# Performance work log

Hardware: AMD Instinct MI355X
Metric: run time of the kernel (lower is better)

## Reference

```python
import jax, jax.numpy as jnp
import numpy as np

VOCAB = 100000
EMB = 300
HID = 512            # bidirectional total; per-direction = 256
HD = HID // 2
TAGS = 12
START = 10
STOP = 11
NEG = -10000.0
T = 4096


def _lstm_dir(x, h0, c0, Wih, Whh, bih, bhh, reverse):
    # x: [T, EMB]; PyTorch gate order i, f, g, o
    def step(carry, xt):
        h, c = carry
        g = xt @ Wih.T + h @ Whh.T + bih + bhh           # [4*HD]
        i, f, gg, o = jnp.split(g, 4)
        i = jax.nn.sigmoid(i); f = jax.nn.sigmoid(f)
        gg = jnp.tanh(gg); o = jax.nn.sigmoid(o)
        c = f * c + i * gg
        h = o * jnp.tanh(c)
        return (h, c), h
    _, hs = jax.lax.scan(step, (h0, c0), x, reverse=reverse)
    return hs                                            # [T, HD]


def setup_inputs() -> dict:
    key = jax.random.key(0)
    ks = jax.random.split(key, 16)
    s = 0.05  # weight scale for numerical stability
    sentence = jax.random.randint(ks[0], (T,), 0, VOCAB)
    h0 = jax.random.normal(ks[1], (2, HD), jnp.float32)
    c0 = jax.random.normal(ks[2], (2, HD), jnp.float32)
    embed = jax.random.normal(ks[3], (VOCAB, EMB), jnp.float32) * s
    W_ih_f = jax.random.normal(ks[4], (4 * HD, EMB), jnp.float32) * s
    W_hh_f = jax.random.normal(ks[5], (4 * HD, HD), jnp.float32) * s
    b_ih_f = jax.random.normal(ks[6], (4 * HD,), jnp.float32) * s
    b_hh_f = jax.random.normal(ks[7], (4 * HD,), jnp.float32) * s
    W_ih_b = jax.random.normal(ks[8], (4 * HD, EMB), jnp.float32) * s
    W_hh_b = jax.random.normal(ks[9], (4 * HD, HD), jnp.float32) * s
    b_ih_b = jax.random.normal(ks[10], (4 * HD,), jnp.float32) * s
    b_hh_b = jax.random.normal(ks[11], (4 * HD,), jnp.float32) * s
    W_tag = jax.random.normal(ks[12], (TAGS, HID), jnp.float32) * s
    b_tag = jax.random.normal(ks[13], (TAGS,), jnp.float32) * s
    transitions = jax.random.normal(ks[14], (TAGS, TAGS), jnp.float32)
    transitions = transitions.at[START, :].set(NEG).at[:, STOP].set(NEG)
    return dict(sentence=sentence, h0=h0, c0=c0, embed=embed,
                W_ih_f=W_ih_f, W_hh_f=W_hh_f, b_ih_f=b_ih_f, b_hh_f=b_hh_f,
                W_ih_b=W_ih_b, W_hh_b=W_hh_b, b_ih_b=b_ih_b, b_hh_b=b_hh_b,
                W_tag=W_tag, b_tag=b_tag, transitions=transitions)


def reference(sentence, h0, c0, embed,
              W_ih_f, W_hh_f, b_ih_f, b_hh_f,
              W_ih_b, W_hh_b, b_ih_b, b_hh_b,
              W_tag, b_tag, transitions):
    # --- BiLSTM features (dropout layers are identity at inference) ---
    x = embed[sentence]                                      # [T, EMB]
    hf = _lstm_dir(x, h0[0], c0[0], W_ih_f, W_hh_f, b_ih_f, b_hh_f, False)
    hb = _lstm_dir(x, h0[1], c0[1], W_ih_b, W_hh_b, b_ih_b, b_hh_b, True)
    feats = jnp.concatenate([hf, hb], axis=-1) @ W_tag.T + b_tag  # [T, TAGS]

    # --- Viterbi decode: transitions[to, from] ---
    init = jnp.full((TAGS,), NEG, jnp.float32).at[START].set(0.0)

    def vstep(fv, feat):
        ntv = fv[None, :] + transitions                      # [to, from]
        bp = jnp.argmax(ntv, axis=1)                         # best prev tag per 'to'
        fv2 = jnp.max(ntv, axis=1) + feat
        return fv2, bp

    fv, bps = jax.lax.scan(vstep, init, feats)               # bps: [T, TAGS]
    terminal = fv + transitions[STOP]
    best = jnp.argmax(terminal)
    path_score = terminal[best]

    def back(tag, bp):
        return bp[tag], tag

    _, best_path = jax.lax.scan(back, best, bps, reverse=True)  # [T] tags in time order
    return path_score, best_path
```

## Files before the change

kernel.cpp:

```cpp
#include <hip/hip_runtime.h>

#define T_LEN 4096
#define EMB   300
#define HD    256
#define G4    1024
#define N2    2048
#define TAGS  12
#define NEGV  -10000.0f
#define SENT  0x7F7F7F7Fu
#define NLSTM 29
#define VCH   512

#define MV(K) { const float4 hv = h4[K];                    \
    a0 = fmaf(wA##K.x, hv.x, a0);                           \
    a1 = fmaf(wA##K.y, hv.y, a1);                           \
    a2 = fmaf(wA##K.z, hv.z, a2);                           \
    a3 = fmaf(wA##K.w, hv.w, a3); }

__global__ __launch_bounds__(1024) void fused_gemm_lstm(
    const int* __restrict__ sent, const float* __restrict__ embed,
    const float* __restrict__ Wihf, const float* __restrict__ Wihb,
    const float* __restrict__ bihf, const float* __restrict__ bhhf,
    const float* __restrict__ bihb, const float* __restrict__ bhhb,
    const float* Whh_f, const float* Whh_b,
    const float* __restrict__ h0, const float* __restrict__ c0,
    float* gin,
    float* Hh)
{
    __shared__ __align__(16) char smem[145*1024];
    const int blk = blockIdx.x;
    const int tid = threadIdx.x;

    if (blk >= NLSTM) {
        float* AsT  = (float*)smem;
        float* BsT  = (float*)(smem + 8704);
        int*   sIdx = (int*)  (smem + 17408);
        const int g  = blk - NLSTM;
        const int kk8 = g >> 5;
        const int bn  = g & 31;
        const int bm  = (kk8 & 1) ? (63 - (kk8 >> 1)) : (kk8 >> 1);

        if (tid < 64) sIdx[tid] = sent[bm*64 + tid];
        __syncthreads();

        const int srow = tid >> 4;
        const int skj  = (tid & 15) << 1;
        const int m0   = (tid >> 5) << 1;
        const int n0   = (tid & 31) << 1;
        const int rn   = bn * 64;
        float acc00=0.f, acc01=0.f, acc10=0.f, acc11=0.f;

        for (int kc = 0; kc < 10; ++kc) {
            const int k0 = kc*32 + skj;
            float2 va = make_float2(0.f, 0.f), vb = make_float2(0.f, 0.f);
            if (k0 + 1 < EMB) {
                va = *(const float2*)(embed + (long)sIdx[srow]*EMB + k0);
                const int r = rn + srow;
                const float* bsrc = (r < G4) ? (Wihf + (long)r*EMB)
                                             : (Wihb + (long)(r-G4)*EMB);
                vb = *(const float2*)(bsrc + k0);
            }
            AsT[skj*68 + srow]     = va.x;
            AsT[(skj+1)*68 + srow] = va.y;
            BsT[skj*68 + srow]     = vb.x;
            BsT[(skj+1)*68 + srow] = vb.y;
            __syncthreads();
            #pragma unroll
            for (int kk = 0; kk < 32; ++kk) {
                const float2 a2v = *(const float2*)&AsT[kk*68 + m0];
                const float2 b2v = *(const float2*)&BsT[kk*68 + n0];
                acc00 = fmaf(a2v.x, b2v.x, acc00);
                acc01 = fmaf(a2v.x, b2v.y, acc01);
                acc10 = fmaf(a2v.y, b2v.x, acc10);
                acc11 = fmaf(a2v.y, b2v.y, acc11);
            }
            __syncthreads();
        }

        const int c0i = rn + n0, c1i = c0i + 1;
        const float bias0 = (c0i < G4) ? (bihf[c0i] + bhhf[c0i])
                                       : (bihb[c0i-G4] + bhhb[c0i-G4]);
        const float bias1 = (c1i < G4) ? (bihf[c1i] + bhhf[c1i])
                                       : (bihb[c1i-G4] + bhhb[c1i-G4]);
        const long t0 = (long)(bm*64 + m0), t1 = t0 + 1;
        __hip_atomic_store(&gin[t0*N2 + c0i], acc00 + bias0,
                           __ATOMIC_RELAXED, __HIP_MEMORY_SCOPE_AGENT);
        __hip_atomic_store(&gin[t0*N2 + c1i], acc01 + bias1,
                           __ATOMIC_RELAXED, __HIP_MEMORY_SCOPE_AGENT);
        __hip_atomic_store(&gin[t1*N2 + c0i], acc10 + bias0,
                           __ATOMIC_RELAXED, __HIP_MEMORY_SCOPE_AGENT);
        __hip_atomic_store(&gin[t1*N2 + c1i], acc11 + bias1,
                           __ATOMIC_RELAXED, __HIP_MEMORY_SCOPE_AGENT);
        return;
    }

    const int m8 = blk & 7;
    if (m8 != 0 && m8 != 4) return;
    const int dir = (m8 == 4);
    const int b   = blk >> 3;
    const int u     = tid & 63;
    const int wvid  = tid >> 6;
    const int gate  = wvid >> 2;
    const int q     = wvid & 3;
    const int unit0 = b*64;
    const int row   = gate*64 + u;
    const int grow  = gate*HD + unit0 + u;

    float* hS  = (float*)smem;
    float* ps  = (float*)(smem + 1024);
    float* gvS = (float*)(smem + 4096);

    const float4* W4 = (const float4*)((dir ? Whh_b : Whh_f)
                                       + (long)grow*HD + q*64);
    const float4 wA0  = W4[0],  wA1  = W4[1],  wA2  = W4[2],  wA3  = W4[3];
    const float4 wA4  = W4[4],  wA5  = W4[5],  wA6  = W4[6],  wA7  = W4[7];
    const float4 wA8  = W4[8],  wA9  = W4[9],  wA10 = W4[10], wA11 = W4[11];
    const float4 wA12 = W4[12], wA13 = W4[13], wA14 = W4[14], wA15 = W4[15];

    float cst = 0.f;
    if (tid < 64) cst = c0[dir*HD + unit0 + tid];
    if (tid < HD) hS[tid] = h0[dir*HD + tid];

    float* ginD = gin + dir*G4;
    float gx;
    {
        const long gi0 = (long)(dir ? T_LEN-1 : 0)*N2 + grow;
        do {
            gx = __hip_atomic_load(&ginD[gi0], __ATOMIC_RELAXED,
                                   __HIP_MEMORY_SCOPE_AGENT);
        } while (__float_as_uint(gx) == SENT);
    }

    #pragma unroll 1
    for (int s = 0; s < T_LEN; ++s) {
        const int t = dir ? (T_LEN-1-s) : s;
        float gxn = 0.f;
        long  gidx = 0;
        if (s+1 < T_LEN) {
            gidx = (long)(dir ? t-1 : t+1)*N2 + grow;
            gxn = __hip_atomic_load(&ginD[gidx], __ATOMIC_RELAXED,
                                    __HIP_MEMORY_SCOPE_AGENT);
            __builtin_amdgcn_sched_barrier(0);
        }

        __syncthreads();
        const float4* h4 = (const float4*)(hS + q*64);
        float a0=0.f, a1=0.f, a2=0.f, a3=0.f;
        MV(0)  MV(1)  MV(2)  MV(3)
        MV(4)  MV(5)  MV(6)  MV(7)
        MV(8)  MV(9)  MV(10) MV(11)
        MV(12) MV(13) MV(14) MV(15)
        const float a = (a0+a1)+(a2+a3);
        if (q != 0) ps[(q-1)*256 + row] = a;
        __syncthreads();

        if (q == 0) {
            const float raw = a + ps[row] + ps[256+row] + ps[512+row] + gx;
            gvS[row] = (gate == 2) ? tanhf(raw) : 1.f/(1.f + expf(-raw));
        }
        __syncthreads();

        if (tid < 64) {
            const float i_ = gvS[tid],       f_ = gvS[64+tid];
            const float g_ = gvS[128+tid],   o_ = gvS[192+tid];
            cst = fmaf(f_, cst, i_*g_);
            const float hv = o_ * tanhf(cst);
            hS[unit0 + tid] = hv;
            __hip_atomic_store(&Hh[(long)t*512 + dir*HD + unit0 + tid], hv,
                               __ATOMIC_RELAXED, __HIP_MEMORY_SCOPE_AGENT);
        } else if (tid < 256 && s+1 < T_LEN) {
            const int fidx = tid - 64;
            const int gu   = (fidx < unit0) ? fidx : fidx + 64;
            const long idx = (long)t*512 + dir*HD + gu;
            float v;
            do {
                v = __hip_atomic_load(&Hh[idx], __ATOMIC_RELAXED,
                                      __HIP_MEMORY_SCOPE_AGENT);
            } while (__float_as_uint(v) == SENT);
            hS[gu] = v;
        }

        if (s+1 < T_LEN) {
            while (__float_as_uint(gxn) == SENT)
                gxn = __hip_atomic_load(&ginD[gidx], __ATOMIC_RELAXED,
                                        __HIP_MEMORY_SCOPE_AGENT);
        }
        gx = gxn;
    }
}

__global__ __launch_bounds__(192) void feats_kernel(
    const float* __restrict__ Hhist, const float* __restrict__ Wtag,
    const float* __restrict__ btag, float* __restrict__ feats)
{
    __shared__ __align__(16) float Ws[TAGS][512];
    const int tid = threadIdx.x;
    for (int i = tid; i < TAGS*512; i += 192) Ws[0][i] = Wtag[i];
    __syncthreads();
    const int tl = tid / TAGS;
    const int tg = tid % TAGS;
    const int t  = blockIdx.x * 16 + tl;
    const float4* hrow = (const float4*)(Hhist + (long)t*512);
    const float4* wrow = (const float4*)(&Ws[tg][0]);
    float a0=0.f,a1=0.f,a2=0.f,a3=0.f;
    #pragma unroll 8
    for (int k = 0; k < 128; ++k) {
        const float4 h = hrow[k];
        const float4 ww = wrow[k];
        a0=fmaf(h.x,ww.x,a0); a1=fmaf(h.y,ww.y,a1);
        a2=fmaf(h.z,ww.z,a2); a3=fmaf(h.w,ww.w,a3);
    }
    feats[t*TAGS + tg] = ((a0+a1)+(a2+a3)) + btag[tg];
}

__global__ __launch_bounds__(64) void viterbi_kernel(
    const float* __restrict__ feats, const float* __restrict__ trans,
    float* __restrict__ fvstore, float* __restrict__ out)
{
    __shared__ __align__(16) float fS[VCH*TAGS];
    __shared__ __align__(16) float fvS[16];
    __shared__ __align__(16) float trS[TAGS*TAGS];
    __shared__ unsigned char bps[T_LEN*TAGS];
    const int lane = threadIdx.x;

    for (int i = lane; i < TAGS*TAGS; i += 64) trS[i] = trans[i];

    const int trow = (lane < TAGS) ? lane : 0;
    float tr[TAGS];
    #pragma unroll
    for (int f = 0; f < TAGS; ++f) tr[f] = trans[trow*TAGS + f];

    float fvv[TAGS];
    #pragma unroll
    for (int f = 0; f < TAGS; ++f) fvv[f] = (f == 10) ? 0.f : NEGV;

    for (int c = 0; c < T_LEN/VCH; ++c) {
        __syncthreads();
        {
            const float4* src = (const float4*)(feats + (long)c*VCH*TAGS);
            float4* dst = (float4*)fS;
            #pragma unroll 4
            for (int i = lane; i < VCH*TAGS/4; i += 64) dst[i] = src[i];
        }
        __syncthreads();
        for (int s = 0; s < VCH; ++s) {
            const int t = c*VCH + s;
            if (lane < TAGS) {
                fvstore[(long)t*TAGS + lane] = fvv[lane];
                float cand[TAGS];
                #pragma unroll
                for (int f = 0; f < TAGS; ++f) cand[f] = fvv[f] + tr[f];
                const float m =
                    fmaxf(fmaxf(fmaxf(fmaxf(cand[0],cand[1]), fmaxf(cand[2],cand[3])),
                                fmaxf(fmaxf(cand[4],cand[5]), fmaxf(cand[6],cand[7]))),
                          fmaxf(fmaxf(cand[8],cand[9]), fmaxf(cand[10],cand[11])));
                fvS[lane] = m + fS[s*TAGS + lane];
            }
            __syncthreads();
            const float4 A = *(const float4*)&fvS[0];
            const float4 B = *(const float4*)&fvS[4];
            const float4 C = *(const float4*)&fvS[8];
            fvv[0]=A.x; fvv[1]=A.y; fvv[2]=A.z; fvv[3]=A.w;
            fvv[4]=B.x; fvv[5]=B.y; fvv[6]=B.z; fvv[7]=B.w;
            fvv[8]=C.x; fvv[9]=C.y; fvv[10]=C.z; fvv[11]=C.w;
            __syncthreads();
        }
    }

    __syncthreads();
    for (int idx = lane; idx < T_LEN*TAGS; idx += 64) {
        const int t  = idx / TAGS;
        const int to = idx - t*TAGS;
        const float* fp = fvstore + (long)t*TAGS;
        float best = -3.4e38f; int bp = 0;
        #pragma unroll
        for (int f = 0; f < TAGS; ++f) {
            const float v = fp[f] + trS[to*TAGS + f];
            if (v > best) { best = v; bp = f; }
        }
        bps[idx] = (unsigned char)bp;
    }
    __syncthreads();

    if (lane == 0) {
        float bestv = -3.4e38f; int best = 0;
        #pragma unroll
        for (int g = 0; g < TAGS; ++g) {
            const float v = fvv[g] + trS[11*TAGS + g];
            if (v > bestv) { bestv = v; best = g; }
        }
        out[0] = bestv;
        int cur = best;
        for (int t = T_LEN-1; t >= 0; --t) {
            out[1+t] = (float)cur;
            cur = bps[t*TAGS + cur];
        }
    }
}

extern "C" void kernel_launch(void* const* d_in, const int* in_sizes, int n_in,
                              void* d_out, int out_size, void* d_ws, size_t ws_size,
                              hipStream_t stream)
{
    (void)in_sizes; (void)n_in; (void)out_size; (void)ws_size;
    const int*   sentence = (const int*)  d_in[0];
    const float* h0       = (const float*)d_in[1];
    const float* c0       = (const float*)d_in[2];
    const float* embed    = (const float*)d_in[3];
    const float* Wihf     = (const float*)d_in[4];
    const float* Whhf     = (const float*)d_in[5];
    const float* bihf     = (const float*)d_in[6];
    const float* bhhf     = (const float*)d_in[7];
    const float* Wihb     = (const float*)d_in[8];
    const float* Whhb     = (const float*)d_in[9];
    const float* bihb     = (const float*)d_in[10];
    const float* bhhb     = (const float*)d_in[11];
    const float* Wtag     = (const float*)d_in[12];
    const float* btag     = (const float*)d_in[13];
    const float* trans    = (const float*)d_in[14];
    float* out = (float*)d_out;

    float* gin     = (float*)d_ws;
    float* Hh      = gin   + (long)T_LEN*N2;
    float* feats   = Hh    + (long)T_LEN*512;
    float* fvstore = feats + (long)T_LEN*TAGS;

    hipMemsetAsync(gin, 0x7F, (size_t)T_LEN*N2*sizeof(float), stream);
    hipMemsetAsync(Hh,  0x7F, (size_t)T_LEN*512*sizeof(float), stream);

    fused_gemm_lstm<<<NLSTM + 2048, 1024, 0, stream>>>(
        sentence, embed, Wihf, Wihb, bihf, bhhf, bihb, bhhb,
        Whhf, Whhb, h0, c0, gin, Hh);
    feats_kernel<<<T_LEN/16, 192, 0, stream>>>(Hh, Wtag, btag, feats);
    viterbi_kernel<<<1, 64, 0, stream>>>(feats, trans, fvstore, out);
}
```

Baseline: 6.815 ms.

## Split LSTM recurrence across eight blocks per direction and reload weights each step

Each direction's recurrent matvec is now spread over 8 cooperating blocks of 32 hidden units instead of 4 blocks of 64. Only 512 of the 1024 threads in each block do work, and NLSTM grows to give the extra blocks. Weights are reloaded from global/L2 after each step, with a sched barrier placed before the cross-block h exchange, so the load latency can overlap the spin-wait. Smaller per-block work shortens the serial critical path per step, but more blocks must synchronise through global memory, which adds polling and exchange cost.

```diff
diff --git a/kernel.cpp b/kernel.cpp
--- a/kernel.cpp
+++ b/kernel.cpp
@@ -8,7 +8,7 @@
 #define TAGS  12
 #define NEGV  -10000.0f
 #define SENT  0x7F7F7F7Fu
-#define NLSTM 29
+#define NLSTM 61
 #define VCH   512
 
 #define MV(K) { const float4 hv = h4[K];                    \
@@ -16,6 +16,11 @@
     a1 = fmaf(wA##K.y, hv.y, a1);                           \
     a2 = fmaf(wA##K.z, hv.z, a2);                           \
     a3 = fmaf(wA##K.w, hv.w, a3); }
+
+#define LOADW { wA0=W4[0]; wA1=W4[1]; wA2=W4[2]; wA3=W4[3];         \
+    wA4=W4[4]; wA5=W4[5]; wA6=W4[6]; wA7=W4[7];                     \
+    wA8=W4[8]; wA9=W4[9]; wA10=W4[10]; wA11=W4[11];                 \
+    wA12=W4[12]; wA13=W4[13]; wA14=W4[14]; wA15=W4[15]; }
 
 __global__ __launch_bounds__(1024) void fused_gemm_lstm(
     const int* __restrict__ sent, const float* __restrict__ embed,
@@ -98,32 +103,31 @@
     if (m8 != 0 && m8 != 4) return;
     const int dir = (m8 == 4);
     const int b   = blk >> 3;
-    const int u     = tid & 63;
-    const int wvid  = tid >> 6;
-    const int gate  = wvid >> 2;
-    const int q     = wvid & 3;
-    const int unit0 = b*64;
-    const int row   = gate*64 + u;
-    const int grow  = gate*HD + unit0 + u;
+    const bool active = (tid < 512);
+    const int q    = (tid >> 7) & 3;
+    const int rl   = tid & 127;
+    const int gate = rl >> 5;
+    const int u    = rl & 31;
+    const int unit0 = b*32;
+    const int unit  = unit0 + u;
+    const int grow  = gate*HD + unit;
 
     float* hS  = (float*)smem;
     float* ps  = (float*)(smem + 1024);
-    float* gvS = (float*)(smem + 4096);
+    float* gvS = (float*)(smem + 2560);
 
     const float4* W4 = (const float4*)((dir ? Whh_b : Whh_f)
                                        + (long)grow*HD + q*64);
-    const float4 wA0  = W4[0],  wA1  = W4[1],  wA2  = W4[2],  wA3  = W4[3];
-    const float4 wA4  = W4[4],  wA5  = W4[5],  wA6  = W4[6],  wA7  = W4[7];
-    const float4 wA8  = W4[8],  wA9  = W4[9],  wA10 = W4[10], wA11 = W4[11];
-    const float4 wA12 = W4[12], wA13 = W4[13], wA14 = W4[14], wA15 = W4[15];
+    float4 wA0,wA1,wA2,wA3,wA4,wA5,wA6,wA7,wA8,wA9,wA10,wA11,wA12,wA13,wA14,wA15;
+    if (active) LOADW;
 
     float cst = 0.f;
-    if (tid < 64) cst = c0[dir*HD + unit0 + tid];
+    if (tid < 32) cst = c0[dir*HD + unit0 + tid];
     if (tid < HD) hS[tid] = h0[dir*HD + tid];
 
     float* ginD = gin + dir*G4;
-    float gx;
-    {
+    float gx = 0.f;
+    if (active && q == 0) {
         const long gi0 = (long)(dir ? T_LEN-1 : 0)*N2 + grow;
         do {
             gx = __hip_atomic_load(&ginD[gi0], __ATOMIC_RELAXED,
@@ -136,7 +140,7 @@
         const int t = dir ? (T_LEN-1-s) : s;
         float gxn = 0.f;
         long  gidx = 0;
-        if (s+1 < T_LEN) {
+        if (active && q == 0 && s+1 < T_LEN) {
             gidx = (long)(dir ? t-1 : t+1)*N2 + grow;
             gxn = __hip_atomic_load(&ginD[gidx], __ATOMIC_RELAXED,
                                     __HIP_MEMORY_SCOPE_AGENT);
@@ -144,33 +148,41 @@
         }
 
         __syncthreads();
-        const float4* h4 = (const float4*)(hS + q*64);
-        float a0=0.f, a1=0.f, a2=0.f, a3=0.f;
-        MV(0)  MV(1)  MV(2)  MV(3)
-        MV(4)  MV(5)  MV(6)  MV(7)
-        MV(8)  MV(9)  MV(10) MV(11)
-        MV(12) MV(13) MV(14) MV(15)
-        const float a = (a0+a1)+(a2+a3);
-        if (q != 0) ps[(q-1)*256 + row] = a;
-        __syncthreads();
-
-        if (q == 0) {
-            const float raw = a + ps[row] + ps[256+row] + ps[512+row] + gx;
-            gvS[row] = (gate == 2) ? tanhf(raw) : 1.f/(1.f + expf(-raw));
-        }
-        __syncthreads();
-
-        if (tid < 64) {
-            const float i_ = gvS[tid],       f_ = gvS[64+tid];
-            const float g_ = gvS[128+tid],   o_ = gvS[192+tid];
+        float a = 0.f;
+        if (active) {
+            const float4* h4 = (const float4*)(hS + q*64);
+            float a0=0.f, a1=0.f, a2=0.f, a3=0.f;
+            MV(0)  MV(1)  MV(2)  MV(3)
+            MV(4)  MV(5)  MV(6)  MV(7)
+            MV(8)  MV(9)  MV(10) MV(11)
+            MV(12) MV(13) MV(14) MV(15)
+            a = (a0+a1)+(a2+a3);
+            if (q != 0) ps[(q-1)*128 + rl] = a;
+        }
+        __syncthreads();
+
+        if (active && q == 0) {
+            const float raw = a + ps[rl] + ps[128+rl] + ps[256+rl] + gx;
+            gvS[rl] = (gate == 2) ? tanhf(raw) : 1.f/(1.f + expf(-raw));
+        }
+        __syncthreads();
+
+        if (tid < 32) {
+            const float i_ = gvS[tid],      f_ = gvS[32+tid];
+            const float g_ = gvS[64+tid],   o_ = gvS[96+tid];
             cst = fmaf(f_, cst, i_*g_);
             const float hv = o_ * tanhf(cst);
             hS[unit0 + tid] = hv;
             __hip_atomic_store(&Hh[(long)t*512 + dir*HD + unit0 + tid], hv,
                                __ATOMIC_RELAXED, __HIP_MEMORY_SCOPE_AGENT);
-        } else if (tid < 256 && s+1 < T_LEN) {
-            const int fidx = tid - 64;
-            const int gu   = (fidx < unit0) ? fidx : fidx + 64;
+        }
+
+        if (active) { LOADW; }
+        __builtin_amdgcn_sched_barrier(0);
+
+        if (tid >= 32 && tid < 256 && s+1 < T_LEN) {
+            const int fid = tid - 32;
+            const int gu  = (fid < unit0) ? fid : fid + 32;
             const long idx = (long)t*512 + dir*HD + gu;
             float v;
             do {
@@ -180,7 +192,7 @@
             hS[gu] = v;
         }
 
-        if (s+1 < T_LEN) {
+        if (active && q == 0 && s+1 < T_LEN) {
             while (__float_as_uint(gxn) == SENT)
                 gxn = __hip_atomic_load(&ginD[gidx], __ATOMIC_RELAXED,
                                         __HIP_MEMORY_SCOPE_AGENT);
```

New measurement: 19.33 ms. +183.7%, slower.

## Fuse tag projection into persistent LSTM kernel and compact LSTM block mapping

Applied to the files above, without the earlier changes.

Moves the hidden-to-tag projection into the fused GEMM/LSTM launch as 64 extra blocks that spin on the sentinel-initialised hidden history and compute features as it arrives, removing a separate kernel launch. The LSTM blocks are renumbered from a sparse (every 8th/4th) layout to contiguous indices, dropping 21 idle blocks. Only the q==0 waves now poll the input-gate buffer. The Viterbi backpointer pass reads each time step's forward vector once as float4s instead of reloading it per tag. The feats blocks spin with sleep and load elements one at a time, so they may compete for CUs or deadlock if they are scheduled before the LSTM blocks.

```diff
diff --git a/kernel.cpp b/kernel.cpp
--- a/kernel.cpp
+++ b/kernel.cpp
@@ -8,7 +8,10 @@
 #define TAGS  12
 #define NEGV  -10000.0f
 #define SENT  0x7F7F7F7Fu
-#define NLSTM 29
+#define NLSTM 8
+#define NGEMM 2048
+#define FEATS0 (NLSTM + NGEMM)
+#define NFEATS 64
 #define VCH   512
 
 #define MV(K) { const float4 hv = h4[K];                    \
@@ -24,12 +27,43 @@
     const float* __restrict__ bihb, const float* __restrict__ bhhb,
     const float* Whh_f, const float* Whh_b,
     const float* __restrict__ h0, const float* __restrict__ c0,
+    const float* __restrict__ Wtag, const float* __restrict__ btag,
     float* gin,
-    float* Hh)
+    float* Hh,
+    float* feats)
 {
     __shared__ __align__(16) char smem[145*1024];
     const int blk = blockIdx.x;
     const int tid = threadIdx.x;
+
+    if (blk >= FEATS0) {
+        float* Ws  = (float*)smem;
+        float* btS = (float*)(smem + 24576);
+        for (int i = tid; i < TAGS*512; i += 1024) Ws[i] = Wtag[i];
+        if (tid < TAGS) btS[tid] = btag[tid];
+        __syncthreads();
+        if (tid < 768) {
+            const int tl = tid / TAGS;
+            const int tg = tid - tl*TAGS;
+            const int t  = (blk - FEATS0)*64 + tl;
+            const float* wrow = Ws + tg*512;
+            float acc = 0.f;
+            for (int k = 0; k < 512; ++k) {
+                float v = __hip_atomic_load(&Hh[(long)t*512 + k],
+                                            __ATOMIC_RELAXED,
+                                            __HIP_MEMORY_SCOPE_AGENT);
+                while (__float_as_uint(v) == SENT) {
+                    __builtin_amdgcn_s_sleep(127);
+                    v = __hip_atomic_load(&Hh[(long)t*512 + k],
+                                          __ATOMIC_RELAXED,
+                                          __HIP_MEMORY_SCOPE_AGENT);
+                }
+                acc = fmaf(v, wrow[k], acc);
+            }
+            feats[t*TAGS + tg] = acc + btS[tg];
+        }
+        return;
+    }
 
     if (blk >= NLSTM) {
         float* AsT  = (float*)smem;
@@ -94,10 +128,8 @@
         return;
     }
 
-    const int m8 = blk & 7;
-    if (m8 != 0 && m8 != 4) return;
-    const int dir = (m8 == 4);
-    const int b   = blk >> 3;
+    const int dir = blk & 1;
+    const int b   = blk >> 1;
     const int u     = tid & 63;
     const int wvid  = tid >> 6;
     const int gate  = wvid >> 2;
@@ -122,8 +154,8 @@
     if (tid < HD) hS[tid] = h0[dir*HD + tid];
 
     float* ginD = gin + dir*G4;
-    float gx;
-    {
+    float gx = 0.f;
+    if (q == 0) {
         const long gi0 = (long)(dir ? T_LEN-1 : 0)*N2 + grow;
         do {
             gx = __hip_atomic_load(&ginD[gi0], __ATOMIC_RELAXED,
@@ -136,7 +168,7 @@
         const int t = dir ? (T_LEN-1-s) : s;
         float gxn = 0.f;
         long  gidx = 0;
-        if (s+1 < T_LEN) {
+        if (q == 0 && s+1 < T_LEN) {
             gidx = (long)(dir ? t-1 : t+1)*N2 + grow;
             gxn = __hip_atomic_load(&ginD[gidx], __ATOMIC_RELAXED,
                                     __HIP_MEMORY_SCOPE_AGENT);
@@ -169,8 +201,8 @@
             __hip_atomic_store(&Hh[(long)t*512 + dir*HD + unit0 + tid], hv,
                                __ATOMIC_RELAXED, __HIP_MEMORY_SCOPE_AGENT);
         } else if (tid < 256 && s+1 < T_LEN) {
-            const int fidx = tid - 64;
-            const int gu   = (fidx < unit0) ? fidx : fidx + 64;
+            const int fid = tid - 64;
+            const int gu  = (fid < unit0) ? fid : fid + 64;
             const long idx = (long)t*512 + dir*HD + gu;
             float v;
             do {
@@ -180,37 +212,13 @@
             hS[gu] = v;
         }
 
-        if (s+1 < T_LEN) {
+        if (q == 0 && s+1 < T_LEN) {
             while (__float_as_uint(gxn) == SENT)
                 gxn = __hip_atomic_load(&ginD[gidx], __ATOMIC_RELAXED,
                                         __HIP_MEMORY_SCOPE_AGENT);
         }
         gx = gxn;
     }
-}
-
-__global__ __launch_bounds__(192) void feats_kernel(
-    const float* __restrict__ Hhist, const float* __restrict__ Wtag,
-    const float* __restrict__ btag, float* __restrict__ feats)
-{
-    __shared__ __align__(16) float Ws[TAGS][512];
-    const int tid = threadIdx.x;
-    for (int i = tid; i < TAGS*512; i += 192) Ws[0][i] = Wtag[i];
-    __syncthreads();
-    const int tl = tid / TAGS;
-    const int tg = tid % TAGS;
-    const int t  = blockIdx.x * 16 + tl;
-    const float4* hrow = (const float4*)(Hhist + (long)t*512);
-    const float4* wrow = (const float4*)(&Ws[tg][0]);
-    float a0=0.f,a1=0.f,a2=0.f,a3=0.f;
-    #pragma unroll 8
-    for (int k = 0; k < 128; ++k) {
-        const float4 h = hrow[k];
-        const float4 ww = wrow[k];
-        a0=fmaf(h.x,ww.x,a0); a1=fmaf(h.y,ww.y,a1);
-        a2=fmaf(h.z,ww.z,a2); a3=fmaf(h.w,ww.w,a3);
-    }
-    feats[t*TAGS + tg] = ((a0+a1)+(a2+a3)) + btag[tg];
 }
 
 __global__ __launch_bounds__(64) void viterbi_kernel(
@@ -268,17 +276,23 @@
     }
 
     __syncthreads();
-    for (int idx = lane; idx < T_LEN*TAGS; idx += 64) {
-        const int t  = idx / TAGS;
-        const int to = idx - t*TAGS;
-        const float* fp = fvstore + (long)t*TAGS;
-        float best = -3.4e38f; int bp = 0;
+    for (int t = lane; t < T_LEN; t += 64) {
+        const float4 F0 = *(const float4*)(fvstore + (long)t*TAGS);
+        const float4 F1 = *(const float4*)(fvstore + (long)t*TAGS + 4);
+        const float4 F2 = *(const float4*)(fvstore + (long)t*TAGS + 8);
+        const float fp[TAGS] = {F0.x,F0.y,F0.z,F0.w,
+                                F1.x,F1.y,F1.z,F1.w,
+                                F2.x,F2.y,F2.z,F2.w};
         #pragma unroll
-        for (int f = 0; f < TAGS; ++f) {
-            const float v = fp[f] + trS[to*TAGS + f];
-            if (v > best) { best = v; bp = f; }
-        }
-        bps[idx] = (unsigned char)bp;
+        for (int to = 0; to < TAGS; ++to) {
+            float best = -3.4e38f; int bp = 0;
+            #pragma unroll
+            for (int f = 0; f < TAGS; ++f) {
+                const float v = fp[f] + trS[to*TAGS + f];
+                if (v > best) { best = v; bp = f; }
+            }
+            bps[t*TAGS + to] = (unsigned char)bp;
+        }
     }
     __syncthreads();
 
@@ -328,9 +342,8 @@
     hipMemsetAsync(gin, 0x7F, (size_t)T_LEN*N2*sizeof(float), stream);
     hipMemsetAsync(Hh,  0x7F, (size_t)T_LEN*512*sizeof(float), stream);
 
-    fused_gemm_lstm<<<NLSTM + 2048, 1024, 0, stream>>>(
+    fused_gemm_lstm<<<FEATS0 + NFEATS, 1024, 0, stream>>>(
         sentence, embed, Wihf, Wihb, bihf, bhhf, bihb, bhhb,
-        Whhf, Whhb, h0, c0, gin, Hh);
-    feats_kernel<<<T_LEN/16, 192, 0, stream>>>(Hh, Wtag, btag, feats);
+        Whhf, Whhb, h0, c0, Wtag, btag, gin, Hh, feats);
     viterbi_kernel<<<1, 64, 0, stream>>>(feats, trans, fvstore, out);
 }
```

Measured after the change: 7.616 ms. 11.7% more time.
